# Kernel optimization log

Hardware: AMD Instinct MI355X
Metric: run time of the kernel (lower is better)

The kernel has to match this reference:

```python
import jax, jax.numpy as jnp
import numpy as np

N_NODES = 50000
N_EDGES = 800000
F_IN, C1, C2 = 128, 100, 4
NEG_SLOPE = 0.2  # PyG GATConv default LeakyReLU slope


def setup_inputs() -> dict:
    key = jax.random.key(0)
    ks = jax.random.split(key, 10)
    def glorot(k, shape):
        fan = sum(shape)
        return jax.random.normal(k, shape, jnp.float32) * jnp.sqrt(2.0 / fan)
    return {
        "x": jax.random.normal(ks[0], (N_NODES, F_IN), jnp.float32),
        "edge_index": jax.random.randint(ks[1], (2, N_EDGES), 0, N_NODES, jnp.int64),
        "W1": glorot(ks[2], (F_IN, C1)),
        "att_src1": glorot(ks[3], (1, C1)),
        "att_dst1": glorot(ks[4], (1, C1)),
        "b1": jnp.zeros((C1,), jnp.float32),
        "W2": glorot(ks[5], (C1, C2)),
        "att_src2": glorot(ks[6], (1, C2)),
        "att_dst2": glorot(ks[7], (1, C2)),
        "b2": jnp.zeros((C2,), jnp.float32),
    }


def _gat_conv(x, edge_index, W, att_src, att_dst, bias):
    """PyG GATConv (heads=1, concat=True, add_self_loops=True), eval mode."""
    n = x.shape[0]
    # add self loops
    loop = jnp.arange(n, dtype=edge_index.dtype)
    src = jnp.concatenate([edge_index[0], loop])
    dst = jnp.concatenate([edge_index[1], loop])
    h = x @ W                                   # [N, C]
    a_src = (h * att_src[0]).sum(-1)            # [N]
    a_dst = (h * att_dst[0]).sum(-1)            # [N]
    e = jax.nn.leaky_relu(a_src[src] + a_dst[dst], NEG_SLOPE)  # [E+N]
    # segment softmax over destination neighborhoods
    m = jax.ops.segment_max(e, dst, num_segments=n)            # [N]
    w = jnp.exp(e - m[dst])
    denom = jax.ops.segment_sum(w, dst, num_segments=n)        # [N]
    alpha = w / denom[dst]                                     # [E+N]
    msg = h[src] * alpha[:, None]                              # [E+N, C]
    out = jax.ops.segment_sum(msg, dst, num_segments=n)        # [N, C]
    return out + bias


def reference(x, edge_index, W1, att_src1, att_dst1, b1, W2, att_src2, att_dst2, b2):
    h = _gat_conv(x, edge_index, W1, att_src1, att_dst1, b1)
    h = jax.nn.relu(h)  # dropout is identity in eval mode
    h = _gat_conv(h, edge_index, W2, att_src2, att_dst2, b2)
    return jax.nn.log_softmax(h, axis=1)
```

## Files before the change

kernel.cpp:

```cpp
#include <hip/hip_runtime.h>
#include <math.h>

#define N_NODES 50000
#define N_EDGES 800000
#define F_IN 128
#define C1 100
#define C1D 50
#define C2 4
#define NEG 0.2f
#define DEGCAP 64
#define NBUCK 196
#define BCAP 4608
#define BSTR 16
#define PA_NB 196
#define PA_CHUNK 1021
#define GEMM_NB 782
#define NB_PREP 56

typedef __attribute__((ext_vector_type(8))) _Float16 f16x8;
typedef __attribute__((ext_vector_type(2))) _Float16 f16x2;
typedef __attribute__((ext_vector_type(4))) float f32x4;

__device__ __forceinline__ float leaky(float v) { return v > 0.f ? v : NEG * v; }

__device__ __forceinline__ unsigned pkh(float a, float b) {
    auto p = __builtin_amdgcn_cvt_pkrtz(a, b);
    return __builtin_bit_cast(unsigned, p);
}
__device__ __forceinline__ float h_lo(unsigned g) {
    f16x2 p = __builtin_bit_cast(f16x2, g);
    return (float)p[0];
}
__device__ __forceinline__ float h_hi(unsigned g) {
    f16x2 p = __builtin_bit_cast(f16x2, g);
    return (float)p[1];
}

__global__ __launch_bounds__(256) void k_prep(int* __restrict__ bcnt, const float* __restrict__ W1,
                                              unsigned short* __restrict__ W1h) {
    int i = blockIdx.x * 256 + threadIdx.x;
    if (i < NBUCK) bcnt[i * BSTR] = 0;
    if (i < 12800) {
        int k = i / 100, n = i - k * 100;
        _Float16 hv = (_Float16)W1[i];
        W1h[n * 128 + k] = __builtin_bit_cast(unsigned short, hv);
    } else if (i < 12800 + 12 * 128) {
        int e = i - 12800;
        int n = 100 + (e >> 7), k = e & 127;
        W1h[n * 128 + k] = 0;
    }
}

__global__ __attribute__((amdgpu_waves_per_eu(1, 3))) __launch_bounds__(256)
void k_gemm_scatter(const float* __restrict__ x, const unsigned short* __restrict__ W1h,
                    const float* __restrict__ as1, const float* __restrict__ ad1,
                    unsigned* __restrict__ h1b, float* __restrict__ a_src1,
                    float* __restrict__ a_dst1, const int* __restrict__ ei,
                    int* __restrict__ bcnt, unsigned* __restrict__ breg) {
    if (blockIdx.x < PA_NB) {
        __shared__ int lcnt[NBUCK];
        __shared__ int lbase[NBUCK];
        int tid = threadIdx.x;
        if (tid < NBUCK) lcnt[tid] = 0;
        __syncthreads();
        int g0 = blockIdx.x * PA_CHUNK;
        int4 s4[4], d4[4];
        int off[4][4];
        bool val[4];
#pragma unroll
        for (int it = 0; it < 4; ++it) {
            int local = it * 256 + tid;
            int g = g0 + local;
            val[it] = (local < PA_CHUNK) && (g < N_EDGES / 4);
            if (val[it]) {
                s4[it] = *(const int4*)(ei + (long)g * 4);
                d4[it] = *(const int4*)(ei + N_EDGES + (long)g * 4);
                off[it][0] = atomicAdd(&lcnt[d4[it].x >> 8], 1);
                off[it][1] = atomicAdd(&lcnt[d4[it].y >> 8], 1);
                off[it][2] = atomicAdd(&lcnt[d4[it].z >> 8], 1);
                off[it][3] = atomicAdd(&lcnt[d4[it].w >> 8], 1);
            }
        }
        __syncthreads();
        if (tid < NBUCK) {
            int c = lcnt[tid];
            lbase[tid] = c ? atomicAdd(&bcnt[tid * BSTR], c) : 0;
        }
        __syncthreads();
#pragma unroll
        for (int it = 0; it < 4; ++it) {
            if (!val[it]) continue;
            { int b = d4[it].x >> 8; int p = lbase[b] + off[it][0];
              if (p < BCAP) breg[b * BCAP + p] = ((unsigned)s4[it].x << 8) | ((unsigned)d4[it].x & 255u); }
            { int b = d4[it].y >> 8; int p = lbase[b] + off[it][1];
              if (p < BCAP) breg[b * BCAP + p] = ((unsigned)s4[it].y << 8) | ((unsigned)d4[it].y & 255u); }
            { int b = d4[it].z >> 8; int p = lbase[b] + off[it][2];
              if (p < BCAP) breg[b * BCAP + p] = ((unsigned)s4[it].z << 8) | ((unsigned)d4[it].z & 255u); }
            { int b = d4[it].w >> 8; int p = lbase[b] + off[it][3];
              if (p < BCAP) breg[b * BCAP + p] = ((unsigned)s4[it].w << 8) | ((unsigned)d4[it].w & 255u); }
        }
        return;
    }
    int half = blockIdx.x - PA_NB;
    int tid = threadIdx.x;
    int node0 = half * 64;
    int wave = tid >> 6, lane = tid & 63;
    int mrow = lane & 15;
    int quad = lane >> 4;
    int na = node0 + wave * 16 + mrow;
    bool vrow = na < N_NODES;
    const float* px = x + (long)na * F_IN + quad * 8;

    f16x8 afr[4];
#pragma unroll
    for (int kc = 0; kc < 4; ++kc) {
        float4 v0 = make_float4(0.f, 0.f, 0.f, 0.f), v1 = v0;
        if (vrow) {
            v0 = *(const float4*)(px + kc * 32);
            v1 = *(const float4*)(px + kc * 32 + 4);
        }
        union { unsigned u[4]; f16x8 h; } t;
        t.u[0] = pkh(v0.x, v0.y);
        t.u[1] = pkh(v0.z, v0.w);
        t.u[2] = pkh(v1.x, v1.y);
        t.u[3] = pkh(v1.z, v1.w);
        afr[kc] = t.h;
    }

    f32x4 acc[7];
#pragma unroll
    for (int nt = 0; nt < 7; ++nt) {
        const _Float16* pb = (const _Float16*)W1h + (nt * 16 + mrow) * 128 + quad * 8;
        f32x4 a = {0.f, 0.f, 0.f, 0.f};
#pragma unroll
        for (int kc = 0; kc < 4; ++kc) {
            f16x8 bfr = *(const f16x8*)(pb + kc * 32);
            a = __builtin_amdgcn_mfma_f32_16x16x32_f16(afr[kc], bfr, a, 0, 0, 0);
        }
        acc[nt] = a;
    }

    float ps[4] = {0.f, 0.f, 0.f, 0.f}, pd[4] = {0.f, 0.f, 0.f, 0.f};
#pragma unroll
    for (int nt = 0; nt < 7; ++nt) {
        int col = nt * 16 + mrow;
        float av = 0.f, dv = 0.f;
        if (col < C1) { av = as1[col]; dv = ad1[col]; }
#pragma unroll
        for (int r = 0; r < 4; ++r) {
            ps[r] += acc[nt][r] * av;
            pd[r] += acc[nt][r] * dv;
        }
    }
#pragma unroll
    for (int r = 0; r < 4; ++r) {
#pragma unroll
        for (int off = 1; off < 16; off <<= 1) {
            ps[r] += __shfl_xor(ps[r], off);
            pd[r] += __shfl_xor(pd[r], off);
        }
    }
    if (mrow == 0) {
#pragma unroll
        for (int r = 0; r < 4; ++r) {
            int n = node0 + wave * 16 + quad * 4 + r;
            if (n < N_NODES) { a_src1[n] = ps[r]; a_dst1[n] = pd[r]; }
        }
    }

#pragma unroll
    for (int nt = 0; nt < 7; ++nt) {
#pragma unroll
        for (int r = 0; r < 4; ++r) {
            float v = acc[nt][r];
            float o = __shfl_xor(v, 1);
            int col = nt * 16 + mrow;
            int n = node0 + wave * 16 + quad * 4 + r;
            if ((mrow & 1) == 0 && col < C1 && n < N_NODES) {
                h1b[(long)n * C1D + (col >> 1)] = pkh(v, o);
            }
        }
    }
}

__global__ __launch_bounds__(512) void k_bucket(const unsigned* __restrict__ breg,
                                                const int* __restrict__ bcnt,
                                                int* __restrict__ cnt,
                                                unsigned short* __restrict__ slots) {
    __shared__ int dcnt[256];
    int b = blockIdx.x, tid = threadIdx.x;
    if (tid < 256) dcnt[tid] = 0;
    __syncthreads();
    int n = min(bcnt[b * BSTR], BCAP);
    const unsigned* reg = breg + b * BCAP;
    for (int e = tid; e < n; e += 512) {
        unsigned p = reg[e];
        int d8 = p & 255;
        int slot = atomicAdd(&dcnt[d8], 1);
        if (slot < DEGCAP) slots[(((b << 8) + d8) << 6) + slot] = (unsigned short)(p >> 8);
    }
    __syncthreads();
    if (tid < 256) {
        int d = (b << 8) + tid;
        if (d < N_NODES) cnt[d] = dcnt[tid];
    }
}

__device__ __forceinline__ float rlanef(float v, int l) {
    return __int_as_float(__builtin_amdgcn_readlane(__float_as_int(v), l));
}

__global__ __launch_bounds__(256) void k_agg1(const unsigned* __restrict__ h1b, const float* __restrict__ a_src,
                                              const float* __restrict__ a_dst, const int* __restrict__ cnt,
                                              const unsigned short* __restrict__ slots, const float* __restrict__ b1,
                                              const float* __restrict__ W2, const float* __restrict__ as2,
                                              const float* __restrict__ ad2, float4* __restrict__ h2,
                                              float* __restrict__ a_src2, float* __restrict__ a_dst2) {
    __shared__ float sW2[C1 * C2];
    __shared__ float sB1[C1];
    int tid = threadIdx.x;
    for (int f = tid; f < C1 * C2; f += 256) sW2[f] = W2[f];
    if (tid < C1) sB1[tid] = b1[tid];
    __syncthreads();
    int wave = tid >> 6, lane = tid & 63;
    int d = blockIdx.x * 4 + wave;
    if (d >= N_NODES) return;
    int cn = min(cnt[d], DEGCAP);
    float ad = a_dst[d];
    int c = lane;
    bool act = c < C1D;
    int cc = act ? c : 0;

    float wself = __expf(leaky(a_src[d] + ad));
    unsigned gs = h1b[(long)d * C1D + cc];
    float accL = wself * h_lo(gs), accH = wself * h_hi(gs);
    float lsum = (lane == 0) ? wself : 0.f;

    int sreg = 0; float wreg = 0.f;
    if (lane < cn) {
        sreg = (int)slots[d * DEGCAP + lane];
        wreg = __expf(leaky(a_src[sreg] + ad));
        lsum += wreg;
    }

    unsigned ga[8], gb[8];
#define LD(buf, e) { int sv_ = __builtin_amdgcn_readlane(sreg, (e)); \
                     buf = h1b[(long)sv_ * C1D + cc]; }
#define CONSUME(buf, e) if ((e) < cn) { float w_ = rlanef(wreg, (e)); \
                     accL = fmaf(h_lo(buf), w_, accL); accH = fmaf(h_hi(buf), w_, accH); }

#pragma unroll
    for (int i = 0; i < 8; ++i) LD(ga[i], i);
#pragma unroll
    for (int bp = 0; bp < 4; ++bp) {
        const int b0 = 2 * bp, b1 = 2 * bp + 1;
        if (b0 * 8 >= cn) break;
        if (b1 * 8 < cn) {
#pragma unroll
            for (int i = 0; i < 8; ++i) LD(gb[i], b1 * 8 + i);
        }
#pragma unroll
        for (int i = 0; i < 8; ++i) CONSUME(ga[i], b0 * 8 + i);
        if (b1 * 8 >= cn) break;
        if ((b1 + 1) * 8 < cn) {
#pragma unroll
            for (int i = 0; i < 8; ++i) LD(ga[i], (b1 + 1) * 8 + i);
        }
#pragma unroll
        for (int i = 0; i < 8; ++i) CONSUME(gb[i], b1 * 8 + i);
    }
#undef LD
#undef CONSUME

    for (int off = 32; off; off >>= 1) lsum += __shfl_xor(lsum, off);
    float invl = 1.f / lsum;
    float p0 = 0.f, p1 = 0.f, p2 = 0.f, p3 = 0.f;
    if (act) {
        float v0 = fmaxf(accL * invl + sB1[2 * c], 0.f);
        float v1 = fmaxf(accH * invl + sB1[2 * c + 1], 0.f);
        const float* w0 = &sW2[(2 * c) * 4];
        p0 = v0 * w0[0] + v1 * w0[4];
        p1 = v0 * w0[1] + v1 * w0[5];
        p2 = v0 * w0[2] + v1 * w0[6];
        p3 = v0 * w0[3] + v1 * w0[7];
    }
    for (int off = 32; off; off >>= 1) {
        p0 += __shfl_xor(p0, off);
        p1 += __shfl_xor(p1, off);
        p2 += __shfl_xor(p2, off);
        p3 += __shfl_xor(p3, off);
    }
    if (lane == 0) {
        h2[d] = make_float4(p0, p1, p2, p3);
        a_src2[d] = p0 * as2[0] + p1 * as2[1] + p2 * as2[2] + p3 * as2[3];
        a_dst2[d] = p0 * ad2[0] + p1 * ad2[1] + p2 * ad2[2] + p3 * ad2[3];
    }
}

__global__ __launch_bounds__(256) void k_agg2(const float4* __restrict__ h2, const float* __restrict__ a_src,
                                              const float* __restrict__ a_dst, const int* __restrict__ cnt,
                                              const unsigned short* __restrict__ slots, const float* __restrict__ b2,
                                              float4* __restrict__ out) {
    int wave = threadIdx.x >> 6, lane = threadIdx.x & 63;
    int grp = lane >> 4, li = lane & 15;
    int d = blockIdx.x * 16 + wave * 4 + grp;
    if (d >= N_NODES) return;
    int cn = min(cnt[d], DEGCAP);
    float ad = a_dst[d];
    float l = 0.f, a0 = 0.f, a1 = 0.f, a2 = 0.f, a3 = 0.f;
    if (li == 0) {
        float w = __expf(leaky(a_src[d] + ad));
        float4 hv = h2[d];
        l = w; a0 = w * hv.x; a1 = w * hv.y; a2 = w * hv.z; a3 = w * hv.w;
    }
    for (int j = li; j < cn; j += 16) {
        int s = (int)slots[d * DEGCAP + j];
        float w = __expf(leaky(a_src[s] + ad));
        l += w;
        float4 hv = h2[s];
        a0 += w * hv.x; a1 += w * hv.y; a2 += w * hv.z; a3 += w * hv.w;
    }
#pragma unroll
    for (int off = 8; off; off >>= 1) {
        l += __shfl_xor(l, off);
        a0 += __shfl_xor(a0, off);
        a1 += __shfl_xor(a1, off);
        a2 += __shfl_xor(a2, off);
        a3 += __shfl_xor(a3, off);
    }
    if (li == 0) {
        float invl = 1.f / l;
        float v0 = a0 * invl + b2[0];
        float v1 = a1 * invl + b2[1];
        float v2 = a2 * invl + b2[2];
        float v3 = a3 * invl + b2[3];
        float mm = fmaxf(fmaxf(v0, v1), fmaxf(v2, v3));
        float ls = logf(__expf(v0 - mm) + __expf(v1 - mm) + __expf(v2 - mm) + __expf(v3 - mm)) + mm;
        out[d] = make_float4(v0 - ls, v1 - ls, v2 - ls, v3 - ls);
    }
}

extern "C" void kernel_launch(void* const* d_in, const int* in_sizes, int n_in,
                              void* d_out, int out_size, void* d_ws, size_t ws_size,
                              hipStream_t stream) {
    const float* x   = (const float*)d_in[0];
    const int*   ei  = (const int*)d_in[1];
    const float* W1  = (const float*)d_in[2];
    const float* as1 = (const float*)d_in[3];
    const float* ad1 = (const float*)d_in[4];
    const float* b1  = (const float*)d_in[5];
    const float* W2  = (const float*)d_in[6];
    const float* as2 = (const float*)d_in[7];
    const float* ad2 = (const float*)d_in[8];
    const float* b2  = (const float*)d_in[9];
    float4* out = (float4*)d_out;

    char* w = (char*)d_ws;
    unsigned* h1b    = (unsigned*)(w + 0);
    float*    a_src1 = (float*)(w + 10000000);
    float*    a_dst1 = (float*)(w + 10200000);
    float4*   h2     = (float4*)(w + 10400000);
    float*    a_src2 = (float*)(w + 11200000);
    float*    a_dst2 = (float*)(w + 11400000);
    int*      cnt    = (int*)(w + 11600000);
    int*      bcnt   = (int*)(w + 11800000);
    unsigned short* slots = (unsigned short*)(w + 11816000);
    unsigned* breg   = (unsigned*)(w + 18216000);
    unsigned short* W1h   = (unsigned short*)(w + 21828672);

    k_prep<<<NB_PREP, 256, 0, stream>>>(bcnt, W1, W1h);
    k_gemm_scatter<<<PA_NB + GEMM_NB, 256, 0, stream>>>(x, W1h, as1, ad1, h1b, a_src1, a_dst1,
                                                        ei, bcnt, breg);
    k_bucket<<<NBUCK, 512, 0, stream>>>(breg, bcnt, cnt, slots);
    k_agg1<<<(N_NODES + 3) / 4, 256, 0, stream>>>(h1b, a_src1, a_dst1, cnt, slots, b1, W2, as2, ad2,
                                                  h2, a_src2, a_dst2);
    k_agg2<<<(N_NODES + 15) / 16, 256, 0, stream>>>(h2, a_src2, a_dst2, cnt, slots, b2, out);
}
```

Before: 165.2 us.

## Fold W1 conversion into GEMM blocks via LDS, pack layer-2 node records

Removes the separate prep kernel. Each GEMM block now converts W1 to fp16 into padded shared memory, and the bucket counters are zeroed with a memset. The layer-2 features and attention scalars are packed into one interleaved 32-byte record per node, so each neighbor gather in agg2 touches adjacent memory. agg2 also switches to a grid-stride loop with a smaller grid. The cost is that every GEMM block redoes the 12.8K-element W1 transpose and conversion, and the larger LDS footprint may lower occupancy.

```diff
diff --git a/kernel.cpp b/kernel.cpp
--- a/kernel.cpp
+++ b/kernel.cpp
@@ -15,7 +15,7 @@
 #define PA_NB 196
 #define PA_CHUNK 1021
 #define GEMM_NB 782
-#define NB_PREP 56
+#define W1P 136
 
 typedef __attribute__((ext_vector_type(8))) _Float16 f16x8;
 typedef __attribute__((ext_vector_type(2))) _Float16 f16x2;
@@ -35,32 +35,24 @@
     f16x2 p = __builtin_bit_cast(f16x2, g);
     return (float)p[1];
 }
-
-__global__ __launch_bounds__(256) void k_prep(int* __restrict__ bcnt, const float* __restrict__ W1,
-                                              unsigned short* __restrict__ W1h) {
-    int i = blockIdx.x * 256 + threadIdx.x;
-    if (i < NBUCK) bcnt[i * BSTR] = 0;
-    if (i < 12800) {
-        int k = i / 100, n = i - k * 100;
-        _Float16 hv = (_Float16)W1[i];
-        W1h[n * 128 + k] = __builtin_bit_cast(unsigned short, hv);
-    } else if (i < 12800 + 12 * 128) {
-        int e = i - 12800;
-        int n = 100 + (e >> 7), k = e & 127;
-        W1h[n * 128 + k] = 0;
-    }
-}
-
-__global__ __attribute__((amdgpu_waves_per_eu(1, 3))) __launch_bounds__(256)
-void k_gemm_scatter(const float* __restrict__ x, const unsigned short* __restrict__ W1h,
+__device__ __forceinline__ float rlanef(float v, int l) {
+    return __int_as_float(__builtin_amdgcn_readlane(__float_as_int(v), l));
+}
+
+__global__ __launch_bounds__(256)
+void k_gemm_scatter(const float* __restrict__ x, const float* __restrict__ W1,
                     const float* __restrict__ as1, const float* __restrict__ ad1,
                     unsigned* __restrict__ h1b, float* __restrict__ a_src1,
                     float* __restrict__ a_dst1, const int* __restrict__ ei,
                     int* __restrict__ bcnt, unsigned* __restrict__ breg) {
+    __shared__ union SM {
+        struct { int lcnt[NBUCK]; int lbase[NBUCK]; } pa;
+        unsigned short w1[112 * W1P];
+    } sm;
+    int tid = threadIdx.x;
     if (blockIdx.x < PA_NB) {
-        __shared__ int lcnt[NBUCK];
-        __shared__ int lbase[NBUCK];
-        int tid = threadIdx.x;
+        int* lcnt = sm.pa.lcnt;
+        int* lbase = sm.pa.lbase;
         if (tid < NBUCK) lcnt[tid] = 0;
         __syncthreads();
         int g0 = blockIdx.x * PA_CHUNK;
@@ -101,8 +93,19 @@
         }
         return;
     }
+    unsigned short* w1s = sm.w1;
+    for (int i = tid; i < 12800; i += 256) {
+        int k = i / 100, n = i - k * 100;
+        _Float16 hv = (_Float16)W1[i];
+        w1s[n * W1P + k] = __builtin_bit_cast(unsigned short, hv);
+    }
+    for (int i = tid; i < 12 * 128; i += 256) {
+        int n = 100 + (i >> 7), k = i & 127;
+        w1s[n * W1P + k] = 0;
+    }
+    __syncthreads();
+
     int half = blockIdx.x - PA_NB;
-    int tid = threadIdx.x;
     int node0 = half * 64;
     int wave = tid >> 6, lane = tid & 63;
     int mrow = lane & 15;
@@ -130,7 +133,7 @@
     f32x4 acc[7];
 #pragma unroll
     for (int nt = 0; nt < 7; ++nt) {
-        const _Float16* pb = (const _Float16*)W1h + (nt * 16 + mrow) * 128 + quad * 8;
+        const _Float16* pb = (const _Float16*)w1s + (nt * 16 + mrow) * W1P + quad * 8;
         f32x4 a = {0.f, 0.f, 0.f, 0.f};
 #pragma unroll
         for (int kc = 0; kc < 4; ++kc) {
@@ -206,16 +209,11 @@
     }
 }
 
-__device__ __forceinline__ float rlanef(float v, int l) {
-    return __int_as_float(__builtin_amdgcn_readlane(__float_as_int(v), l));
-}
-
 __global__ __launch_bounds__(256) void k_agg1(const unsigned* __restrict__ h1b, const float* __restrict__ a_src,
                                               const float* __restrict__ a_dst, const int* __restrict__ cnt,
                                               const unsigned short* __restrict__ slots, const float* __restrict__ b1,
                                               const float* __restrict__ W2, const float* __restrict__ as2,
-                                              const float* __restrict__ ad2, float4* __restrict__ h2,
-                                              float* __restrict__ a_src2, float* __restrict__ a_dst2) {
+                                              const float* __restrict__ ad2, float4* __restrict__ recs) {
     __shared__ float sW2[C1 * C2];
     __shared__ float sB1[C1];
     int tid = threadIdx.x;
@@ -253,21 +251,21 @@
     for (int i = 0; i < 8; ++i) LD(ga[i], i);
 #pragma unroll
     for (int bp = 0; bp < 4; ++bp) {
-        const int b0 = 2 * bp, b1 = 2 * bp + 1;
+        const int b0 = 2 * bp, b1i = 2 * bp + 1;
         if (b0 * 8 >= cn) break;
-        if (b1 * 8 < cn) {
-#pragma unroll
-            for (int i = 0; i < 8; ++i) LD(gb[i], b1 * 8 + i);
+        if (b1i * 8 < cn) {
+#pragma unroll
+            for (int i = 0; i < 8; ++i) LD(gb[i], b1i * 8 + i);
         }
 #pragma unroll
         for (int i = 0; i < 8; ++i) CONSUME(ga[i], b0 * 8 + i);
-        if (b1 * 8 >= cn) break;
-        if ((b1 + 1) * 8 < cn) {
-#pragma unroll
-            for (int i = 0; i < 8; ++i) LD(ga[i], (b1 + 1) * 8 + i);
-        }
-#pragma unroll
-        for (int i = 0; i < 8; ++i) CONSUME(gb[i], b1 * 8 + i);
+        if (b1i * 8 >= cn) break;
+        if ((b1i + 1) * 8 < cn) {
+#pragma unroll
+            for (int i = 0; i < 8; ++i) LD(ga[i], (b1i + 1) * 8 + i);
+        }
+#pragma unroll
+        for (int i = 0; i < 8; ++i) CONSUME(gb[i], b1i * 8 + i);
     }
 #undef LD
 #undef CONSUME
@@ -291,52 +289,54 @@
         p3 += __shfl_xor(p3, off);
     }
     if (lane == 0) {
-        h2[d] = make_float4(p0, p1, p2, p3);
-        a_src2[d] = p0 * as2[0] + p1 * as2[1] + p2 * as2[2] + p3 * as2[3];
-        a_dst2[d] = p0 * ad2[0] + p1 * ad2[1] + p2 * ad2[2] + p3 * ad2[3];
-    }
-}
-
-__global__ __launch_bounds__(256) void k_agg2(const float4* __restrict__ h2, const float* __restrict__ a_src,
-                                              const float* __restrict__ a_dst, const int* __restrict__ cnt,
+        recs[2 * d] = make_float4(p0, p1, p2, p3);
+        float s2 = p0 * as2[0] + p1 * as2[1] + p2 * as2[2] + p3 * as2[3];
+        float t2 = p0 * ad2[0] + p1 * ad2[1] + p2 * ad2[2] + p3 * ad2[3];
+        recs[2 * d + 1] = make_float4(s2, t2, 0.f, 0.f);
+    }
+}
+
+__global__ __launch_bounds__(256) void k_agg2(const float4* __restrict__ recs, const int* __restrict__ cnt,
                                               const unsigned short* __restrict__ slots, const float* __restrict__ b2,
                                               float4* __restrict__ out) {
     int wave = threadIdx.x >> 6, lane = threadIdx.x & 63;
     int grp = lane >> 4, li = lane & 15;
-    int d = blockIdx.x * 16 + wave * 4 + grp;
-    if (d >= N_NODES) return;
-    int cn = min(cnt[d], DEGCAP);
-    float ad = a_dst[d];
-    float l = 0.f, a0 = 0.f, a1 = 0.f, a2 = 0.f, a3 = 0.f;
-    if (li == 0) {
-        float w = __expf(leaky(a_src[d] + ad));
-        float4 hv = h2[d];
-        l = w; a0 = w * hv.x; a1 = w * hv.y; a2 = w * hv.z; a3 = w * hv.w;
-    }
-    for (int j = li; j < cn; j += 16) {
-        int s = (int)slots[d * DEGCAP + j];
-        float w = __expf(leaky(a_src[s] + ad));
-        l += w;
-        float4 hv = h2[s];
-        a0 += w * hv.x; a1 += w * hv.y; a2 += w * hv.z; a3 += w * hv.w;
-    }
-#pragma unroll
-    for (int off = 8; off; off >>= 1) {
-        l += __shfl_xor(l, off);
-        a0 += __shfl_xor(a0, off);
-        a1 += __shfl_xor(a1, off);
-        a2 += __shfl_xor(a2, off);
-        a3 += __shfl_xor(a3, off);
-    }
-    if (li == 0) {
-        float invl = 1.f / l;
-        float v0 = a0 * invl + b2[0];
-        float v1 = a1 * invl + b2[1];
-        float v2 = a2 * invl + b2[2];
-        float v3 = a3 * invl + b2[3];
-        float mm = fmaxf(fmaxf(v0, v1), fmaxf(v2, v3));
-        float ls = logf(__expf(v0 - mm) + __expf(v1 - mm) + __expf(v2 - mm) + __expf(v3 - mm)) + mm;
-        out[d] = make_float4(v0 - ls, v1 - ls, v2 - ls, v3 - ls);
+    for (int d = blockIdx.x * 16 + wave * 4 + grp; d < N_NODES; d += gridDim.x * 16) {
+        int cn = min(cnt[d], DEGCAP);
+        float ad = recs[2 * d + 1].y;
+        float l = 0.f, a0 = 0.f, a1 = 0.f, a2 = 0.f, a3 = 0.f;
+        if (li == 0) {
+            float4 r1 = recs[2 * d + 1];
+            float w = __expf(leaky(r1.x + ad));
+            float4 hv = recs[2 * d];
+            l = w; a0 = w * hv.x; a1 = w * hv.y; a2 = w * hv.z; a3 = w * hv.w;
+        }
+        for (int j = li; j < cn; j += 16) {
+            int s = (int)slots[d * DEGCAP + j];
+            float4 r1 = recs[2 * s + 1];
+            float w = __expf(leaky(r1.x + ad));
+            l += w;
+            float4 hv = recs[2 * s];
+            a0 += w * hv.x; a1 += w * hv.y; a2 += w * hv.z; a3 += w * hv.w;
+        }
+#pragma unroll
+        for (int off = 8; off; off >>= 1) {
+            l += __shfl_xor(l, off);
+            a0 += __shfl_xor(a0, off);
+            a1 += __shfl_xor(a1, off);
+            a2 += __shfl_xor(a2, off);
+            a3 += __shfl_xor(a3, off);
+        }
+        if (li == 0) {
+            float invl = 1.f / l;
+            float v0 = a0 * invl + b2[0];
+            float v1 = a1 * invl + b2[1];
+            float v2 = a2 * invl + b2[2];
+            float v3 = a3 * invl + b2[3];
+            float mm = fmaxf(fmaxf(v0, v1), fmaxf(v2, v3));
+            float ls = logf(__expf(v0 - mm) + __expf(v1 - mm) + __expf(v2 - mm) + __expf(v3 - mm)) + mm;
+            out[d] = make_float4(v0 - ls, v1 - ls, v2 - ls, v3 - ls);
+        }
     }
 }
 
@@ -359,20 +359,17 @@
     unsigned* h1b    = (unsigned*)(w + 0);
     float*    a_src1 = (float*)(w + 10000000);
     float*    a_dst1 = (float*)(w + 10200000);
-    float4*   h2     = (float4*)(w + 10400000);
-    float*    a_src2 = (float*)(w + 11200000);
-    float*    a_dst2 = (float*)(w + 11400000);
-    int*      cnt    = (int*)(w + 11600000);
-    int*      bcnt   = (int*)(w + 11800000);
-    unsigned short* slots = (unsigned short*)(w + 11816000);
-    unsigned* breg   = (unsigned*)(w + 18216000);
-    unsigned short* W1h   = (unsigned short*)(w + 21828672);
-
-    k_prep<<<NB_PREP, 256, 0, stream>>>(bcnt, W1, W1h);
-    k_gemm_scatter<<<PA_NB + GEMM_NB, 256, 0, stream>>>(x, W1h, as1, ad1, h1b, a_src1, a_dst1,
+    float4*   recs   = (float4*)(w + 10400000);
+    int*      cnt    = (int*)(w + 12000000);
+    int*      bcnt   = (int*)(w + 12200000);
+    unsigned short* slots = (unsigned short*)(w + 12216000);
+    unsigned* breg   = (unsigned*)(w + 18616000);
+
+    hipMemsetAsync(bcnt, 0, NBUCK * BSTR * 4, stream);
+    k_gemm_scatter<<<PA_NB + GEMM_NB, 256, 0, stream>>>(x, W1, as1, ad1, h1b, a_src1, a_dst1,
                                                         ei, bcnt, breg);
     k_bucket<<<NBUCK, 512, 0, stream>>>(breg, bcnt, cnt, slots);
     k_agg1<<<(N_NODES + 3) / 4, 256, 0, stream>>>(h1b, a_src1, a_dst1, cnt, slots, b1, W2, as2, ad2,
-                                                  h2, a_src2, a_dst2);
-    k_agg2<<<(N_NODES + 15) / 16, 256, 0, stream>>>(h2, a_src2, a_dst2, cnt, slots, b2, out);
-}
+                                                  recs);
+    k_agg2<<<1563, 256, 0, stream>>>(recs, cnt, slots, b2, out);
+}
```

Result: faster. 155.3 us (-6.0%).
